# Kernel tuning notes

Hardware: AMD Instinct MI355X
Metric: run time of the kernel (lower is better)

## Reference

```python
import jax, jax.numpy as jnp
import numpy as np
from jax import lax

D_MODEL = 2048
D_STATE = 16
D_CONV = 4
D_INNER = 4096   # expand * d_model
DT_RANK = 128    # ceil(d_model / 16)
BATCH = 4
SEQLEN = 2048


def setup_inputs() -> dict:
    key = jax.random.key(0)
    ks = jax.random.split(key, 8)
    rnd = lambda k, shape, s: jax.random.normal(k, shape, dtype=jnp.float32) * s
    hidden_states = rnd(ks[0], (BATCH, SEQLEN, D_MODEL), 1.0)
    in_proj_w = rnd(ks[1], (2 * D_INNER, D_MODEL), D_MODEL ** -0.5)
    conv_w = rnd(ks[2], (D_INNER, 1, D_CONV), 0.3)
    conv_b = rnd(ks[3], (D_INNER,), 0.1)
    x_proj_w = rnd(ks[4], (DT_RANK + 2 * D_STATE, D_INNER), D_INNER ** -0.5)
    dt_proj_w = rnd(ks[5], (D_INNER, DT_RANK), DT_RANK ** -0.5)
    dt_proj_b = rnd(ks[6], (D_INNER,), 0.5) - 2.0  # bias dt small, like mamba dt init
    out_proj_w = rnd(ks[7], (D_MODEL, D_INNER), D_INNER ** -0.5)
    # A init: -exp(log(arange(1..N))) broadcast over channels -> (d_state, d_inner)
    A = -jnp.tile(jnp.arange(1, D_STATE + 1, dtype=jnp.float32)[:, None], (1, D_INNER))
    D = jnp.ones((D_INNER,), dtype=jnp.float32)
    conv_state = jnp.zeros((BATCH, D_INNER, D_CONV), jnp.float32)
    ssm_state = jnp.zeros((BATCH, D_STATE, D_INNER), jnp.float32)
    last_token_ids = jnp.full((BATCH,), SEQLEN, dtype=jnp.int32)
    return dict(hidden_states=hidden_states, last_token_ids=last_token_ids,
                conv_state=conv_state, ssm_state=ssm_state,
                remove_padding=False, batch_size=BATCH,
                in_proj_w=in_proj_w, conv_w=conv_w, conv_b=conv_b,
                x_proj_w=x_proj_w, dt_proj_w=dt_proj_w, dt_proj_b=dt_proj_b,
                A=A, D=D, out_proj_w=out_proj_w)


def _mamba_forward(hidden_states, in_proj_w, conv_w, conv_b, x_proj_w,
                   dt_proj_w, dt_proj_b, A, D, out_proj_w):
    b, L, _ = hidden_states.shape
    # in_proj (no bias)
    xz = jnp.einsum('bld,ed->ble', hidden_states, in_proj_w)          # (b, L, 2*d_inner)
    x, z = jnp.split(xz, 2, axis=-1)
    x_bdl = x.transpose(0, 2, 1)                                       # (b, d_inner, L)
    # present conv state = last d_conv columns of pre-conv x (F.pad with negative pad)
    new_conv_state = x_bdl[:, :, L - D_CONV:]
    # causal depthwise conv1d (left pad d_conv-1 == pad-both then truncate to L)
    x_conv = lax.conv_general_dilated(
        x_bdl, conv_w, window_strides=(1,), padding=[(D_CONV - 1, 0)],
        feature_group_count=D_INNER,
        dimension_numbers=('NCH', 'OIH', 'NCH')) + conv_b[None, :, None]
    u = jax.nn.silu(x_conv).transpose(0, 2, 1)                          # (b, L, d_inner)
    # x_proj -> dt, B, C
    x_dbl = jnp.einsum('bld,ed->ble', u, x_proj_w)
    dt, Bm, Cm = jnp.split(x_dbl, [DT_RANK, DT_RANK + D_STATE], axis=-1)
    dt = jnp.einsum('blr,dr->bld', dt, dt_proj_w)                       # no bias here
    # selective scan (delta_bias=dt_proj_b, delta_softplus=True)
    delta = jax.nn.softplus(dt + dt_proj_b)                             # (b, L, d_inner)
    dBu = delta * u                                                     # (b, L, d_inner)

    def step(x_state, inp):
        d_i, bu_i, B_i, C_i = inp                                       # (b,d),(b,d),(b,n),(b,n)
        dA = jnp.exp(d_i[:, None, :] * A[None])                         # (b, n, d)
        x_state = dA * x_state + B_i[:, :, None] * bu_i[:, None, :]
        y = jnp.einsum('bnd,bn->bd', x_state, C_i)
        return x_state, y

    x0 = jnp.zeros((b, D_STATE, D_INNER), jnp.float32)
    xs = (delta.transpose(1, 0, 2), dBu.transpose(1, 0, 2),
          Bm.transpose(1, 0, 2), Cm.transpose(1, 0, 2))
    last_state, ys = lax.scan(step, x0, xs)
    y = ys.transpose(1, 0, 2) + u * D                                   # + D skip
    y = y * jax.nn.silu(z)                                              # gate
    out = jnp.einsum('bld,ed->ble', y, out_proj_w)                      # out_proj (no bias)
    return out, new_conv_state, last_state


def reference(hidden_states, last_token_ids, conv_state, ssm_state,
              remove_padding, batch_size,
              in_proj_w, conv_w, conv_b, x_proj_w, dt_proj_w, dt_proj_b,
              A, D, out_proj_w):
    # remove_padding=False and last_token_ids all == L: the torch per-sequence
    # loop is exactly one batched forward_impl with seqlen_offset=0.
    return _mamba_forward(hidden_states, in_proj_w, conv_w, conv_b, x_proj_w,
                          dt_proj_w, dt_proj_b, A, D, out_proj_w)
```

## Files before the change

kernel.cpp:

```cpp
#include <hip/hip_runtime.h>
#include <hip/hip_bf16.h>
#include <math.h>

typedef __attribute__((ext_vector_type(4))) float fvec4;
typedef __attribute__((ext_vector_type(2))) float fvec2;
typedef __attribute__((ext_vector_type(4))) int ivec4;
typedef __attribute__((ext_vector_type(4))) unsigned short usvec4;
typedef __attribute__((ext_vector_type(8))) short bf16x8;

#define SEQ 2048
#define DMODEL 2048
#define DINNER 4096
#define DSTATE 16
#define DTRANK 128
#define NB 4
#define MROWS (NB*SEQ)
#define NCHUNK 16
#define LC (SEQ/NCHUNK)

__device__ __forceinline__ float bf2f(unsigned short h){
  union{unsigned int u; float f;} v; v.u = ((unsigned int)h)<<16; return v.f;
}
__device__ __forceinline__ unsigned short f2bf(float f){
  union{float f; unsigned int u;} v; v.f=f;
  unsigned int r = v.u + 0x7fffu + ((v.u>>16)&1u);
  return (unsigned short)(r>>16);
}
__device__ __forceinline__ void async16(const void* g, void* l){
  __builtin_amdgcn_global_load_lds((const __attribute__((address_space(1))) void*)g,
                                   (__attribute__((address_space(3))) void*)l, 16, 0, 0);
}
__device__ __forceinline__ float sigf(float x){ return 1.f/(1.f+__expf(-x)); }

__device__ __forceinline__ void cvt4(const float* s, unsigned short* d, int i){
  fvec4 v = *(const fvec4*)(s + i);
  usvec4 o;
  o[0]=f2bf(v[0]); o[1]=f2bf(v[1]); o[2]=f2bf(v[2]); o[3]=f2bf(v[3]);
  *(usvec4*)(d + i) = o;
}

__global__ void cvt2_kernel(const float* __restrict__ a, unsigned short* __restrict__ oa,
                            const float* __restrict__ b, unsigned short* __restrict__ ob, int n){
  int i = (blockIdx.x*256 + threadIdx.x)*4;
  if (i < n) cvt4(a, oa, i);
  else       cvt4(b, ob, i - n);
}
__global__ void cvt3_kernel(const float* __restrict__ a, unsigned short* __restrict__ oa, int na,
                            const float* __restrict__ b, unsigned short* __restrict__ ob, int nb,
                            const float* __restrict__ c, unsigned short* __restrict__ oc, int nc){
  int i = (blockIdx.x*256 + threadIdx.x)*4;
  if (i < na){ cvt4(a, oa, i); return; }
  i -= na;
  if (i < nb){ cvt4(b, ob, i); return; }
  i -= nb;
  if (i < nc) cvt4(c, oc, i);
}

template<int MODE>
__global__ __launch_bounds__(512, 2) void gemm256(
    const unsigned short* __restrict__ A,
    const unsigned short* __restrict__ B,
    int K, int nbx, int ldc,
    unsigned short* __restrict__ Cb1,
    unsigned short* __restrict__ Cb2,
    float* __restrict__ Cf,
    const float* __restrict__ bias)
{
  __shared__ __align__(16) unsigned short lds[65536];
  char* ldsc = (char*)lds;
  const int t = threadIdx.x;

  const int nwg = gridDim.x;
  const int cpx = nwg >> 3;
  const int bid = blockIdx.x;
  const int swzb = (bid & 7)*cpx + (bid >> 3);
  const int bx = swzb % nbx, by = swzb / nbx;

  const int bA0 = t*16, bA1 = 8192 + t*16;
  const int sw0 = bA0 ^ (((bA0>>7)&3)<<4);
  const int sw1 = bA1 ^ (((bA1>>7)&3)<<4);
  const int gr0 = sw0>>6, gc0 = (sw0&63)>>1;
  const int gr1 = sw1>>6, gc1 = (sw1&63)>>1;
  const unsigned short* Ab = A + (long)by*256*K;
  const unsigned short* Bb = B + (long)bx*256*K;
  const unsigned short* gA0 = Ab + (long)gr0*K + gc0;
  const unsigned short* gA1 = Ab + (long)gr1*K + gc1;
  const unsigned short* gB0 = Bb + (long)gr0*K + gc0;
  const unsigned short* gB1 = Bb + (long)gr1*K + gc1;

  const int wid = t>>6, lane = t&63;
  const int wm = wid>>2, wn = wid&3;
  const int fr = lane&15, fc = lane>>4;
  const int cb = (fc<<4) ^ (((fr>>1)&3)<<4);
  const int offA = (wm*128 + fr)*64 + cb;
  const int offB = 16384 + (wn*64 + fr)*64 + cb;

  fvec4 acc[8][4];
  #pragma unroll
  for (int i=0;i<8;i++){
    #pragma unroll
    for (int j=0;j<4;j++) acc[i][j] = (fvec4)(0.f);
  }

  const int NKT = K >> 5;
  auto stage = [&](int slot, int k0){
    char* sb = ldsc + slot*32768;
    async16(gA0 + k0, sb + t*16);
    async16(gA1 + k0, sb + 8192 + t*16);
    async16(gB0 + k0, sb + 16384 + t*16);
    async16(gB1 + k0, sb + 24576 + t*16);
  };

  stage(0, 0); stage(1, 32); stage(2, 64);

  bf16x8 aP[4], aQ[4], bU[4], bV[4];
  asm volatile("s_waitcnt vmcnt(8)" ::: "memory");
  __builtin_amdgcn_s_barrier();
  __builtin_amdgcn_sched_barrier(0);
  #pragma unroll
  for (int i=0;i<4;i++) aP[i] = *(const bf16x8*)(ldsc + offA + i*1024);
  #pragma unroll
  for (int j=0;j<4;j++) bU[j] = *(const bf16x8*)(ldsc + offB + j*1024);

#define GEM_HALF(KT, BC, BN) { \
    const char* cs = ldsc + ((KT)&3)*32768; \
    const char* ns = ldsc + (((KT)+1)&3)*32768; \
    asm volatile("s_waitcnt vmcnt(4)" ::: "memory"); \
    __builtin_amdgcn_s_barrier(); \
    __builtin_amdgcn_sched_barrier(0); \
    { int ks = (KT) + 3; if (ks > NKT-1) ks = NKT-1; stage(((KT)+3)&3, ks*32); } \
    __builtin_amdgcn_sched_barrier(0); \
    _Pragma("unroll") \
    for (int i=0;i<4;i++) aQ[i] = *(const bf16x8*)(cs + offA + (4+i)*1024); \
    __builtin_amdgcn_s_setprio(1); \
    _Pragma("unroll") \
    for (int i=0;i<4;i++){ \
      _Pragma("unroll") \
      for (int j=0;j<4;j++) \
        acc[i][j] = __builtin_amdgcn_mfma_f32_16x16x32_bf16(aP[i], BC[j], acc[i][j], 0,0,0); \
    } \
    __builtin_amdgcn_s_setprio(0); \
    _Pragma("unroll") \
    for (int i=0;i<4;i++) aP[i] = *(const bf16x8*)(ns + offA + i*1024); \
    _Pragma("unroll") \
    for (int j=0;j<4;j++) BN[j] = *(const bf16x8*)(ns + offB + j*1024); \
    __builtin_amdgcn_s_setprio(1); \
    _Pragma("unroll") \
    for (int i=0;i<4;i++){ \
      _Pragma("unroll") \
      for (int j=0;j<4;j++) \
        acc[4+i][j] = __builtin_amdgcn_mfma_f32_16x16x32_bf16(aQ[i], BC[j], acc[4+i][j], 0,0,0); \
    } \
    __builtin_amdgcn_s_setprio(0); \
  }

  for (int kt = 0; kt < NKT; kt += 2){
    GEM_HALF(kt,   bU, bV);
    GEM_HALF(kt+1, bV, bU);
  }
#undef GEM_HALF

  const long crow0 = (long)by*256 + wm*128;
  const int  ccol0 = bx*256 + wn*64;
  float bs[4];
  if (MODE==2){
    #pragma unroll
    for (int j=0;j<4;j++) bs[j] = bias[ccol0 + j*16 + fr];
  }
  #pragma unroll
  for (int i=0;i<8;i++){
    #pragma unroll
    for (int j=0;j<4;j++){
      #pragma unroll
      for (int q=0;q<4;q++){
        long rg = crow0 + i*16 + fc*4 + q;
        int  cg = ccol0 + j*16 + fr;
        float v = acc[i][j][q];
        if (MODE==0){
          if (cg < DINNER) Cb1[rg*DINNER + cg] = f2bf(v);
          else             Cb2[rg*DINNER + (cg-DINNER)] = f2bf(v);
        } else if (MODE==2){
          float x = v + bs[j];
          float sp = (x > 20.f) ? x : log1pf(__expf(x));
          Cb1[rg*(long)ldc + cg] = f2bf(sp);
        } else {
          Cf[rg*(long)ldc + cg] = v;
        }
      }
    }
  }
}

template<int MODE>
__global__ __launch_bounds__(256) void gemm_bt(
    const unsigned short* __restrict__ A,
    const unsigned short* __restrict__ B,
    int lda, int Kloop, int Nreal,
    float* __restrict__ Cf,
    int ldc)
{
  __shared__ __align__(16) unsigned short As[128*32];
  __shared__ __align__(16) unsigned short Bs[128*32];
  const int t = threadIdx.x;
  const int bx = blockIdx.x, by = blockIdx.y;
  const long koff = (long)blockIdx.z * Kloop;
  const int wave = t>>6, lane = t&63;
  const int wr = (wave>>1)*64, wc = (wave&1)*64;
  const int fr = lane&15, fc = lane>>4;
  fvec4 acc[4][4];
  #pragma unroll
  for(int i=0;i<4;i++){
    #pragma unroll
    for(int j=0;j<4;j++){ acc[i][j] = (fvec4)(0.f); }
  }
  const int srow = t>>2;
  const int scol = (t&3)*8;
  long rowA = (long)by*128 + srow;
  int rB0 = bx*128 + srow;      if (rB0 > Nreal-1) rB0 = Nreal-1;
  int rB1 = bx*128 + 64 + srow; if (rB1 > Nreal-1) rB1 = Nreal-1;
  const unsigned short* gA0 = A + rowA*(long)lda + scol + koff;
  const unsigned short* gA1 = gA0 + 64L*lda;
  const unsigned short* gB0 = B + (long)rB0*lda + scol + koff;
  const unsigned short* gB1 = B + (long)rB1*lda + scol + koff;
  unsigned short* lA0 = &As[t*8];
  unsigned short* lA1 = &As[2048 + t*8];
  unsigned short* lB0 = &Bs[t*8];
  unsigned short* lB1 = &Bs[2048 + t*8];

  for (int k0 = 0; k0 < Kloop; k0 += 32){
    async16(gA0 + k0, lA0);
    async16(gA1 + k0, lA1);
    async16(gB0 + k0, lB0);
    async16(gB1 + k0, lB1);
    __syncthreads();
    bf16x8 af[4], bv[4];
    #pragma unroll
    for(int i=0;i<4;i++){
      af[i] = *(const bf16x8*)&As[(wr + i*16 + fr)*32 + fc*8];
      bv[i] = *(const bf16x8*)&Bs[(wc + i*16 + fr)*32 + fc*8];
    }
    #pragma unroll
    for(int i=0;i<4;i++){
      #pragma unroll
      for(int j=0;j<4;j++){
        acc[i][j] = __builtin_amdgcn_mfma_f32_16x16x32_bf16(af[i], bv[j], acc[i][j], 0,0,0);
      }
    }
    __syncthreads();
  }

  const long crow0 = (long)by*128 + wr;
  const int ccol0 = bx*128 + wc;
  float* Cfz = Cf + (long)blockIdx.z * MROWS * ldc;
  #pragma unroll
  for(int i=0;i<4;i++){
    #pragma unroll
    for(int j=0;j<4;j++){
      #pragma unroll
      for(int q=0;q<4;q++){
        long rg = crow0 + i*16 + fc*4 + q;
        int  cg = ccol0 + j*16 + fr;
        if (cg < Nreal) Cfz[rg*ldc + cg] = acc[i][j][q];
      }
    }
  }
}

__global__ void reduce_xproj(const float* __restrict__ part,
                             float* __restrict__ xdbl,
                             unsigned short* __restrict__ dtr){
  int i = blockIdx.x*256 + threadIdx.x;
  long base = (long)i*4;
  fvec4 s = *(const fvec4*)&part[base];
  #pragma unroll
  for (int z=1; z<4; z++){
    fvec4 p = *(const fvec4*)&part[(long)z*MROWS*160 + base];
    s[0]+=p[0]; s[1]+=p[1]; s[2]+=p[2]; s[3]+=p[3];
  }
  *(fvec4*)&xdbl[base] = s;
  long mrow = base / 160;
  int c = (int)(base - mrow*160);
  if (c < DTRANK){
    usvec4 o; o[0]=f2bf(s[0]); o[1]=f2bf(s[1]); o[2]=f2bf(s[2]); o[3]=f2bf(s[3]);
    *(usvec4*)&dtr[mrow*DTRANK + c] = o;
  }
}

__global__ __launch_bounds__(256) void conv_silu_kernel(
    const unsigned short* __restrict__ xb, const float* __restrict__ w,
    const float* __restrict__ bias, unsigned short* __restrict__ ub,
    float* __restrict__ cs_out)
{
  int gid = blockIdx.x*256 + threadIdx.x;
  int d0 = (gid & 511)*8;
  long m = gid >> 9;
  int l = (int)(m & (SEQ-1));
  fvec4 w4[8];
  #pragma unroll
  for(int k=0;k<8;k++) w4[k] = *(const fvec4*)&w[(d0+k)*4];
  float acc[8];
  fvec4 b0 = *(const fvec4*)&bias[d0];
  fvec4 b1 = *(const fvec4*)&bias[d0+4];
  acc[0]=b0[0];acc[1]=b0[1];acc[2]=b0[2];acc[3]=b0[3];
  acc[4]=b1[0];acc[5]=b1[1];acc[6]=b1[2];acc[7]=b1[3];
  float xcur[8];
  #pragma unroll
  for(int j=0;j<4;j++){
    int lj = l-3+j;
    if (lj >= 0){
      ivec4 xv = *(const ivec4*)&xb[(m-3+j)*DINNER + d0];
      float xs[8];
      #pragma unroll
      for(int q=0;q<4;q++){
        unsigned int wd = (unsigned int)xv[q];
        xs[2*q]   = bf2f((unsigned short)(wd & 0xffffu));
        xs[2*q+1] = bf2f((unsigned short)(wd >> 16));
      }
      #pragma unroll
      for(int k=0;k<8;k++) acc[k] += xs[k]*w4[k][j];
      if (j==3){
        #pragma unroll
        for(int k=0;k<8;k++) xcur[k] = xs[k];
      }
    }
  }
  if (l >= SEQ-4){
    int b = (int)(m >> 11);
    int jj = l - (SEQ-4);
    #pragma unroll
    for(int k=0;k<8;k++) cs_out[b*16384 + (d0+k)*4 + jj] = xcur[k];
  }
  ivec4 ov;
  #pragma unroll
  for(int q=0;q<4;q++){
    float y0 = acc[2*q]  * sigf(acc[2*q]);
    float y1 = acc[2*q+1]* sigf(acc[2*q+1]);
    ov[q] = (int)((unsigned)f2bf(y0) | ((unsigned)f2bf(y1) << 16));
  }
  *(ivec4*)&ub[m*DINNER + d0] = ov;
}

__device__ __forceinline__ void exp_powers(float dl, float* e){
  float e1 = __expf(-dl);
  float p2 = e1*e1, p3 = p2*e1, p4 = p2*p2;
  float p5 = p4*e1, p6 = p4*p2, p7 = p4*p3, p8 = p4*p4;
  e[0]=e1; e[1]=p2; e[2]=p3; e[3]=p4; e[4]=p5; e[5]=p6; e[6]=p7; e[7]=p8;
  e[8]=p8*e1; e[9]=p8*p2; e[10]=p8*p3; e[11]=p8*p4;
  e[12]=p8*p5; e[13]=p8*p6; e[14]=p8*p7; e[15]=p8*p8;
}

__global__ __launch_bounds__(256) void scan_part1(
    const unsigned short* __restrict__ delta_b,
    const unsigned short* __restrict__ u_b,
    const float* __restrict__ xdbl,
    const float* __restrict__ Amat,
    float* __restrict__ S,
    float* __restrict__ sdelta)
{
  const int t = threadIdx.x;
  const int blk = blockIdx.x;
  const int c = blk & 15, b = (blk>>4)&3, d = (blk>>6)*256 + t;
  float a[16], s[16];
  #pragma unroll
  for (int n=0;n<16;n++){ a[n] = Amat[n*DINNER+d]; s[n]=0.f; }
  bool powA = true;
  #pragma unroll
  for (int n=0;n<16;n++) powA = powA && (a[n] == -(float)(n+1));
  float sd = 0.f;
  const long mbase = (long)b*SEQ + c*LC;

#define S1_BODY(EXPR_E) \
  for (int l=0;l<LC;l++){ \
    long m = mbase + l; \
    float dl = bf2f(delta_b[m*DINNER+d]); \
    float ul = bf2f(u_b[m*DINNER+d]); \
    const float* xb = &xdbl[m*160 + 128]; \
    float dbu = dl*ul; \
    sd += dl; \
    float e[16]; EXPR_E; \
    _Pragma("unroll") \
    for (int g=0; g<4; g++){ \
      fvec4 Bg = *(const fvec4*)(xb + 4*g); \
      _Pragma("unroll") \
      for (int q=0;q<4;q++){ \
        int n = g*4+q; \
        s[n] = e[n]*s[n] + Bg[q]*dbu; \
      } \
    } \
  }

  if (powA){
    S1_BODY(exp_powers(dl, e))
  } else {
    S1_BODY({ _Pragma("unroll") for (int n=0;n<16;n++) e[n] = __expf(dl*a[n]); })
  }
#undef S1_BODY

  const long base = ((long)(b*NCHUNK + c)*DSTATE)*DINNER + d;
  #pragma unroll
  for (int n=0;n<16;n++) S[base + (long)n*DINNER] = s[n];
  sdelta[(long)(b*NCHUNK+c)*DINNER + d] = sd;
}

__global__ __launch_bounds__(256) void scan_part2(
    const float* __restrict__ S,
    const float* __restrict__ sdelta,
    const float* __restrict__ Amat,
    float* __restrict__ Xin,
    float* __restrict__ last_state)
{
  int id = blockIdx.x*256 + threadIdx.x;
  int d = id & (DINNER-1);
  int n = (id>>12) & 15;
  int b = id>>16;
  float a = Amat[n*DINNER+d];
  float X = 0.f;
  #pragma unroll
  for (int c=0;c<NCHUNK;c++){
    long sb = ((long)(b*NCHUNK+c)*DSTATE + n)*DINNER + d;
    Xin[sb] = X;
    float sd = sdelta[(long)(b*NCHUNK+c)*DINNER + d];
    float Sc = S[sb];
    X = __expf(a*sd)*X + Sc;
  }
  last_state[((long)b*DSTATE + n)*DINNER + d] = X;
}

__global__ __launch_bounds__(256) void scan_part3(
    const unsigned short* __restrict__ delta_b,
    const unsigned short* __restrict__ u_b,
    const unsigned short* __restrict__ z_b,
    const float* __restrict__ xdbl,
    const float* __restrict__ Amat,
    const float* __restrict__ Dvec,
    const float* __restrict__ Xin,
    unsigned short* __restrict__ y_b)
{
  const int t = threadIdx.x;
  const int blk = blockIdx.x;
  const int c = blk & 15, b = (blk>>4)&3, d = (blk>>6)*256 + t;
  float a[16], s[16];
  const long xb0 = ((long)(b*NCHUNK + c)*DSTATE)*DINNER + d;
  #pragma unroll
  for (int n=0;n<16;n++){
    a[n] = Amat[n*DINNER+d];
    s[n] = Xin[xb0 + (long)n*DINNER];
  }
  bool powA = true;
  #pragma unroll
  for (int n=0;n<16;n++) powA = powA && (a[n] == -(float)(n+1));
  const float Dd = Dvec[d];
  const long mbase = (long)b*SEQ + c*LC;

#define S3_BODY(EXPR_E) \
  for (int l=0;l<LC;l++){ \
    long m = mbase + l; \
    float dl = bf2f(delta_b[m*DINNER+d]); \
    float ul = bf2f(u_b[m*DINNER+d]); \
    float zl = bf2f(z_b[m*DINNER+d]); \
    const float* xb = &xdbl[m*160 + 128]; \
    float dbu = dl*ul; \
    float y = 0.f; \
    float e[16]; EXPR_E; \
    _Pragma("unroll") \
    for (int g=0; g<4; g++){ \
      fvec4 Bg = *(const fvec4*)(xb + 4*g); \
      fvec4 Cg = *(const fvec4*)(xb + 16 + 4*g); \
      _Pragma("unroll") \
      for (int q=0;q<4;q++){ \
        int n = g*4+q; \
        s[n] = e[n]*s[n] + Bg[q]*dbu; \
        y += Cg[q]*s[n]; \
      } \
    } \
    float yy = y + ul*Dd; \
    float zs = zl*sigf(zl); \
    y_b[m*DINNER+d] = f2bf(yy*zs); \
  }

  if (powA){
    S3_BODY(exp_powers(dl, e))
  } else {
    S3_BODY({ _Pragma("unroll") for (int n=0;n<16;n++) e[n] = __expf(dl*a[n]); })
  }
#undef S3_BODY
}

extern "C" void kernel_launch(void* const* d_in, const int* in_sizes, int n_in,
                              void* d_out, int out_size, void* d_ws, size_t ws_size,
                              hipStream_t stream) {
  const float* hs     = (const float*)d_in[0];
  const float* w_in   = (const float*)d_in[6];
  const float* conv_w = (const float*)d_in[7];
  const float* conv_b = (const float*)d_in[8];
  const float* w_xp   = (const float*)d_in[9];
  const float* w_dt   = (const float*)d_in[10];
  const float* dt_bias= (const float*)d_in[11];
  const float* Amat   = (const float*)d_in[12];
  const float* Dvec   = (const float*)d_in[13];
  const float* w_out  = (const float*)d_in[14];
  float* out = (float*)d_out;

  char* ws = (char*)d_ws;
  const size_t MiB = (size_t)1 << 20;

  unsigned short *hs_b, *w_in_b, *x_b, *z_b, *u_b, *delta_b;
  unsigned short *wxp_b, *wdt_b, *wout_b, *dtr_b, *y_b;
  float *xdbl, *Sbuf, *Xin, *sdelta, *xpart;

  if (ws_size >= 424*MiB){
    size_t off = 0;
    auto alloc = [&](size_t bytes)->void*{ void* p = ws + off; off += (bytes + 255) & ~(size_t)255; return p; };
    hs_b   = (unsigned short*)alloc((size_t)MROWS*DMODEL*2);
    w_in_b = (unsigned short*)alloc((size_t)2*DINNER*DMODEL*2);
    x_b    = (unsigned short*)alloc((size_t)MROWS*DINNER*2);
    z_b    = (unsigned short*)alloc((size_t)MROWS*DINNER*2);
    u_b    = (unsigned short*)alloc((size_t)MROWS*DINNER*2);
    delta_b= (unsigned short*)alloc((size_t)MROWS*DINNER*2);
    wxp_b  = (unsigned short*)alloc((size_t)160*DINNER*2);
    wdt_b  = (unsigned short*)alloc((size_t)DINNER*DTRANK*2);
    wout_b = (unsigned short*)alloc((size_t)DMODEL*DINNER*2);
    xdbl   = (float*)alloc((size_t)MROWS*160*4);
    dtr_b  = (unsigned short*)alloc((size_t)MROWS*DTRANK*2);
    Sbuf   = (float*)alloc((size_t)NB*NCHUNK*DSTATE*DINNER*4);
    Xin    = (float*)alloc((size_t)NB*NCHUNK*DSTATE*DINNER*4);
    sdelta = (float*)alloc((size_t)NB*NCHUNK*DINNER*4);
    xpart  = (float*)alloc((size_t)4*MROWS*160*4);
    y_b    = x_b;
  } else {
    hs_b    = (unsigned short*)(ws + 0);
    w_in_b  = (unsigned short*)(ws + 32*MiB);
    xpart   = (float*)         (ws + 0);
    delta_b = (unsigned short*)(ws + 0);
    x_b     = (unsigned short*)(ws + 64*MiB);
    wxp_b   = (unsigned short*)(ws + 64*MiB);
    wdt_b   = (unsigned short*)(ws + 66*MiB);
    wout_b  = (unsigned short*)(ws + 68*MiB);
    xdbl    = (float*)         (ws + 84*MiB);
    dtr_b   = (unsigned short*)(ws + 90*MiB);
    Sbuf    = (float*)         (ws + 92*MiB);
    Xin     = (float*)         (ws + 108*MiB);
    sdelta  = (float*)         (ws + 124*MiB);
    z_b     = (unsigned short*)(ws + 128*MiB);
    u_b     = (unsigned short*)(ws + 192*MiB);
    y_b     = u_b;
  }

  cvt2_kernel<<<(2*MROWS*DMODEL)/1024, 256, 0, stream>>>(hs, hs_b, w_in, w_in_b,
                                                         MROWS*DMODEL);
  gemm256<0><<<1024, 512, 0, stream>>>(hs_b, w_in_b, DMODEL, 32, 0,
                                       x_b, z_b, nullptr, nullptr);
  conv_silu_kernel<<<(MROWS*512)/256, 256, 0, stream>>>(x_b, conv_w, conv_b, u_b,
                                                        out + (size_t)MROWS*DMODEL);
  {
    int na = 160*DINNER, nb = DINNER*DTRANK, nc = DMODEL*DINNER;
    int tot4 = (na+nb+nc)/4;
    cvt3_kernel<<<(tot4+255)/256, 256, 0, stream>>>(w_xp, wxp_b, na,
                                                    w_dt, wdt_b, nb,
                                                    w_out, wout_b, nc);
  }
  gemm_bt<4><<<dim3(2,64,4), 256, 0, stream>>>(u_b, wxp_b, DINNER, 1024, 160,
                                               xpart, 160);
  reduce_xproj<<<(MROWS*160/4)/256, 256, 0, stream>>>(xpart, xdbl, dtr_b);
  gemm256<2><<<512, 512, 0, stream>>>(dtr_b, wdt_b, DTRANK, 16, DINNER,
                                      delta_b, nullptr, nullptr, dt_bias);
  scan_part1<<<1024, 256, 0, stream>>>(delta_b, u_b, xdbl, Amat, Sbuf, sdelta);
  scan_part2<<<1024, 256, 0, stream>>>(Sbuf, sdelta, Amat, Xin,
                                       out + (size_t)MROWS*DMODEL + NB*DINNER*4);
  scan_part3<<<1024, 256, 0, stream>>>(delta_b, u_b, z_b, xdbl, Amat, Dvec, Xin, y_b);
  gemm256<3><<<256, 512, 0, stream>>>(y_b, wout_b, DINNER, 8, DMODEL,
                                      nullptr, nullptr, out, nullptr);
}
```

Baseline: 862.7 us.

## Switch big GEMM to BK=64 double-buffered LDS and move dt_proj to small-tile GEMM

The 256x256 GEMM changes from a 4-slot, 32-wide K ring with a prefetch depth of three to two 64-wide K slots with a new 128-byte-row XOR swizzle. It now waits for all loads (vmcnt(0)) before each tile, so prefetch depth drops to one in exchange for fewer barriers per K. The dt_proj GEMM (K=128, softplus epilogue) moves from gemm256 to the 128x128 gemm_bt kernel, which now takes a MODE==2 bias/softplus epilogue. This gives more blocks for that small-K GEMM. The shallower pipeline risks exposing global-load latency in the large in_proj and out_proj GEMMs.

```diff
diff --git a/kernel.cpp b/kernel.cpp
--- a/kernel.cpp
+++ b/kernel.cpp
@@ -3,7 +3,6 @@
 #include <math.h>
 
 typedef __attribute__((ext_vector_type(4))) float fvec4;
-typedef __attribute__((ext_vector_type(2))) float fvec2;
 typedef __attribute__((ext_vector_type(4))) int ivec4;
 typedef __attribute__((ext_vector_type(4))) unsigned short usvec4;
 typedef __attribute__((ext_vector_type(8))) short bf16x8;
@@ -63,8 +62,7 @@
     int K, int nbx, int ldc,
     unsigned short* __restrict__ Cb1,
     unsigned short* __restrict__ Cb2,
-    float* __restrict__ Cf,
-    const float* __restrict__ bias)
+    float* __restrict__ Cf)
 {
   __shared__ __align__(16) unsigned short lds[65536];
   char* ldsc = (char*)lds;
@@ -76,24 +74,19 @@
   const int swzb = (bid & 7)*cpx + (bid >> 3);
   const int bx = swzb % nbx, by = swzb / nbx;
 
-  const int bA0 = t*16, bA1 = 8192 + t*16;
-  const int sw0 = bA0 ^ (((bA0>>7)&3)<<4);
-  const int sw1 = bA1 ^ (((bA1>>7)&3)<<4);
-  const int gr0 = sw0>>6, gc0 = (sw0&63)>>1;
-  const int gr1 = sw1>>6, gc1 = (sw1&63)>>1;
-  const unsigned short* Ab = A + (long)by*256*K;
-  const unsigned short* Bb = B + (long)bx*256*K;
-  const unsigned short* gA0 = Ab + (long)gr0*K + gc0;
-  const unsigned short* gA1 = Ab + (long)gr1*K + gc1;
-  const unsigned short* gB0 = Bb + (long)gr0*K + gc0;
-  const unsigned short* gB1 = Bb + (long)gr1*K + gc1;
+  const int r0 = t>>3;
+  const int cel = ((t&7) ^ (r0&7)) * 8;
+  const unsigned short* gA = A + (long)by*256*K + (long)r0*K + cel;
+  const unsigned short* gB = B + (long)bx*256*K + (long)r0*K + cel;
+  const long P64 = 64L*K;
 
   const int wid = t>>6, lane = t&63;
   const int wm = wid>>2, wn = wid&3;
   const int fr = lane&15, fc = lane>>4;
-  const int cb = (fc<<4) ^ (((fr>>1)&3)<<4);
-  const int offA = (wm*128 + fr)*64 + cb;
-  const int offB = 16384 + (wn*64 + fr)*64 + cb;
+  const int x0 = ((fc ^ (fr&7))<<4);
+  const int x1 = (((4+fc) ^ (fr&7))<<4);
+  const int arow = (wm*128 + fr)*128;
+  const int brow = 32768 + (wn*64 + fr)*128;
 
   fvec4 acc[8][4];
   #pragma unroll
@@ -102,71 +95,71 @@
     for (int j=0;j<4;j++) acc[i][j] = (fvec4)(0.f);
   }
 
-  const int NKT = K >> 5;
+  const int NKT = K >> 6;
   auto stage = [&](int slot, int k0){
-    char* sb = ldsc + slot*32768;
-    async16(gA0 + k0, sb + t*16);
-    async16(gA1 + k0, sb + 8192 + t*16);
-    async16(gB0 + k0, sb + 16384 + t*16);
-    async16(gB1 + k0, sb + 24576 + t*16);
+    char* sb = ldsc + slot*65536;
+    #pragma unroll
+    for (int p=0;p<4;p++) async16(gA + p*P64 + k0, sb + p*8192 + t*16);
+    #pragma unroll
+    for (int p=0;p<4;p++) async16(gB + p*P64 + k0, sb + 32768 + p*8192 + t*16);
   };
 
-  stage(0, 0); stage(1, 32); stage(2, 64);
+  stage(0, 0);
 
   bf16x8 aP[4], aQ[4], bU[4], bV[4];
-  asm volatile("s_waitcnt vmcnt(8)" ::: "memory");
-  __builtin_amdgcn_s_barrier();
-  __builtin_amdgcn_sched_barrier(0);
-  #pragma unroll
-  for (int i=0;i<4;i++) aP[i] = *(const bf16x8*)(ldsc + offA + i*1024);
-  #pragma unroll
-  for (int j=0;j<4;j++) bU[j] = *(const bf16x8*)(ldsc + offB + j*1024);
-
-#define GEM_HALF(KT, BC, BN) { \
-    const char* cs = ldsc + ((KT)&3)*32768; \
-    const char* ns = ldsc + (((KT)+1)&3)*32768; \
-    asm volatile("s_waitcnt vmcnt(4)" ::: "memory"); \
-    __builtin_amdgcn_s_barrier(); \
-    __builtin_amdgcn_sched_barrier(0); \
-    { int ks = (KT) + 3; if (ks > NKT-1) ks = NKT-1; stage(((KT)+3)&3, ks*32); } \
-    __builtin_amdgcn_sched_barrier(0); \
-    _Pragma("unroll") \
-    for (int i=0;i<4;i++) aQ[i] = *(const bf16x8*)(cs + offA + (4+i)*1024); \
-    __builtin_amdgcn_s_setprio(1); \
-    _Pragma("unroll") \
-    for (int i=0;i<4;i++){ \
-      _Pragma("unroll") \
-      for (int j=0;j<4;j++) \
-        acc[i][j] = __builtin_amdgcn_mfma_f32_16x16x32_bf16(aP[i], BC[j], acc[i][j], 0,0,0); \
-    } \
-    __builtin_amdgcn_s_setprio(0); \
-    _Pragma("unroll") \
-    for (int i=0;i<4;i++) aP[i] = *(const bf16x8*)(ns + offA + i*1024); \
-    _Pragma("unroll") \
-    for (int j=0;j<4;j++) BN[j] = *(const bf16x8*)(ns + offB + j*1024); \
-    __builtin_amdgcn_s_setprio(1); \
-    _Pragma("unroll") \
-    for (int i=0;i<4;i++){ \
-      _Pragma("unroll") \
-      for (int j=0;j<4;j++) \
-        acc[4+i][j] = __builtin_amdgcn_mfma_f32_16x16x32_bf16(aQ[i], BC[j], acc[4+i][j], 0,0,0); \
-    } \
-    __builtin_amdgcn_s_setprio(0); \
-  }
-
-  for (int kt = 0; kt < NKT; kt += 2){
-    GEM_HALF(kt,   bU, bV);
-    GEM_HALF(kt+1, bV, bU);
-  }
-#undef GEM_HALF
+  for (int kt = 0; kt < NKT; ++kt){
+    const char* cs = ldsc + (kt&1)*65536;
+    asm volatile("s_waitcnt vmcnt(0)" ::: "memory");
+    __builtin_amdgcn_s_barrier();
+    __builtin_amdgcn_sched_barrier(0);
+    if (kt+1 < NKT) stage((kt+1)&1, (kt+1)*64);
+    __builtin_amdgcn_sched_barrier(0);
+    #pragma unroll
+    for (int i=0;i<4;i++) aP[i] = *(const bf16x8*)(cs + arow + i*2048 + x0);
+    #pragma unroll
+    for (int j=0;j<4;j++) bU[j] = *(const bf16x8*)(cs + brow + j*2048 + x0);
+    #pragma unroll
+    for (int i=0;i<4;i++) aQ[i] = *(const bf16x8*)(cs + arow + (4+i)*2048 + x0);
+    __builtin_amdgcn_s_setprio(1);
+    #pragma unroll
+    for (int i=0;i<4;i++){
+      #pragma unroll
+      for (int j=0;j<4;j++)
+        acc[i][j] = __builtin_amdgcn_mfma_f32_16x16x32_bf16(aP[i], bU[j], acc[i][j], 0,0,0);
+    }
+    __builtin_amdgcn_s_setprio(0);
+    #pragma unroll
+    for (int i=0;i<4;i++) aP[i] = *(const bf16x8*)(cs + arow + i*2048 + x1);
+    #pragma unroll
+    for (int j=0;j<4;j++) bV[j] = *(const bf16x8*)(cs + brow + j*2048 + x1);
+    __builtin_amdgcn_s_setprio(1);
+    #pragma unroll
+    for (int i=0;i<4;i++){
+      #pragma unroll
+      for (int j=0;j<4;j++)
+        acc[4+i][j] = __builtin_amdgcn_mfma_f32_16x16x32_bf16(aQ[i], bU[j], acc[4+i][j], 0,0,0);
+    }
+    __builtin_amdgcn_s_setprio(0);
+    #pragma unroll
+    for (int i=0;i<4;i++) aQ[i] = *(const bf16x8*)(cs + arow + (4+i)*2048 + x1);
+    __builtin_amdgcn_s_setprio(1);
+    #pragma unroll
+    for (int i=0;i<4;i++){
+      #pragma unroll
+      for (int j=0;j<4;j++)
+        acc[i][j] = __builtin_amdgcn_mfma_f32_16x16x32_bf16(aP[i], bV[j], acc[i][j], 0,0,0);
+    }
+    #pragma unroll
+    for (int i=0;i<4;i++){
+      #pragma unroll
+      for (int j=0;j<4;j++)
+        acc[4+i][j] = __builtin_amdgcn_mfma_f32_16x16x32_bf16(aQ[i], bV[j], acc[4+i][j], 0,0,0);
+    }
+    __builtin_amdgcn_s_setprio(0);
+  }
 
   const long crow0 = (long)by*256 + wm*128;
   const int  ccol0 = bx*256 + wn*64;
-  float bs[4];
-  if (MODE==2){
-    #pragma unroll
-    for (int j=0;j<4;j++) bs[j] = bias[ccol0 + j*16 + fr];
-  }
   #pragma unroll
   for (int i=0;i<8;i++){
     #pragma unroll
@@ -179,10 +172,6 @@
         if (MODE==0){
           if (cg < DINNER) Cb1[rg*DINNER + cg] = f2bf(v);
           else             Cb2[rg*DINNER + (cg-DINNER)] = f2bf(v);
-        } else if (MODE==2){
-          float x = v + bs[j];
-          float sp = (x > 20.f) ? x : log1pf(__expf(x));
-          Cb1[rg*(long)ldc + cg] = f2bf(sp);
         } else {
           Cf[rg*(long)ldc + cg] = v;
         }
@@ -197,13 +186,15 @@
     const unsigned short* __restrict__ B,
     int lda, int Kloop, int Nreal,
     float* __restrict__ Cf,
+    unsigned short* __restrict__ Cb1,
+    const float* __restrict__ bias,
     int ldc)
 {
   __shared__ __align__(16) unsigned short As[128*32];
   __shared__ __align__(16) unsigned short Bs[128*32];
   const int t = threadIdx.x;
   const int bx = blockIdx.x, by = blockIdx.y;
-  const long koff = (long)blockIdx.z * Kloop;
+  const long koff = (MODE==4) ? (long)blockIdx.z * Kloop : 0;
   const int wave = t>>6, lane = t&63;
   const int wr = (wave>>1)*64, wc = (wave&1)*64;
   const int fr = lane&15, fc = lane>>4;
@@ -251,7 +242,7 @@
 
   const long crow0 = (long)by*128 + wr;
   const int ccol0 = bx*128 + wc;
-  float* Cfz = Cf + (long)blockIdx.z * MROWS * ldc;
+  float* Cfz = (MODE==4) ? (Cf + (long)blockIdx.z * MROWS * ldc) : Cf;
   #pragma unroll
   for(int i=0;i<4;i++){
     #pragma unroll
@@ -260,7 +251,14 @@
       for(int q=0;q<4;q++){
         long rg = crow0 + i*16 + fc*4 + q;
         int  cg = ccol0 + j*16 + fr;
-        if (cg < Nreal) Cfz[rg*ldc + cg] = acc[i][j][q];
+        float v = acc[i][j][q];
+        if (MODE==4){
+          if (cg < Nreal) Cfz[rg*ldc + cg] = v;
+        } else if (MODE==2){
+          float x = v + bias[cg];
+          float sp = (x > 20.f) ? x : log1pf(__expf(x));
+          Cb1[rg*ldc + cg] = f2bf(sp);
+        }
       }
     }
   }
@@ -549,7 +547,7 @@
   cvt2_kernel<<<(2*MROWS*DMODEL)/1024, 256, 0, stream>>>(hs, hs_b, w_in, w_in_b,
                                                          MROWS*DMODEL);
   gemm256<0><<<1024, 512, 0, stream>>>(hs_b, w_in_b, DMODEL, 32, 0,
-                                       x_b, z_b, nullptr, nullptr);
+                                       x_b, z_b, nullptr);
   conv_silu_kernel<<<(MROWS*512)/256, 256, 0, stream>>>(x_b, conv_w, conv_b, u_b,
                                                         out + (size_t)MROWS*DMODEL);
   {
@@ -560,14 +558,14 @@
                                                     w_out, wout_b, nc);
   }
   gemm_bt<4><<<dim3(2,64,4), 256, 0, stream>>>(u_b, wxp_b, DINNER, 1024, 160,
-                                               xpart, 160);
+                                               xpart, nullptr, nullptr, 160);
   reduce_xproj<<<(MROWS*160/4)/256, 256, 0, stream>>>(xpart, xdbl, dtr_b);
-  gemm256<2><<<512, 512, 0, stream>>>(dtr_b, wdt_b, DTRANK, 16, DINNER,
-                                      delta_b, nullptr, nullptr, dt_bias);
+  gemm_bt<2><<<dim3(32,64), 256, 0, stream>>>(dtr_b, wdt_b, DTRANK, DTRANK, DINNER,
+                                              nullptr, delta_b, dt_bias, DINNER);
   scan_part1<<<1024, 256, 0, stream>>>(delta_b, u_b, xdbl, Amat, Sbuf, sdelta);
   scan_part2<<<1024, 256, 0, stream>>>(Sbuf, sdelta, Amat, Xin,
                                        out + (size_t)MROWS*DMODEL + NB*DINNER*4);
   scan_part3<<<1024, 256, 0, stream>>>(delta_b, u_b, z_b, xdbl, Amat, Dvec, Xin, y_b);
   gemm256<3><<<256, 512, 0, stream>>>(y_b, wout_b, DINNER, 8, DMODEL,
-                                      nullptr, nullptr, out, nullptr);
-}
+                                      nullptr, nullptr, out);
+}
```

Result: faster. 829.1 us (-3.9%).
